# Optimization experiments

Hardware: AMD Instinct MI355X
Metric: run time of the kernel (lower is better)

## Reference

```python
import jax, jax.numpy as jnp
import numpy as np

N_NODES = 50000
IN_C = 128
OUT_C = 128
N_EDGES = 1600000
NEG_SLOPE = 0.2
EPS = 1e-16  # matches torch_geometric softmax denominator epsilon


def setup_inputs() -> dict:
    key = jax.random.key(0)
    k1, k2, k3, k4, k5 = jax.random.split(key, 5)
    glorot = 1.0 / np.sqrt(IN_C)
    x = jax.random.normal(k1, (N_NODES, IN_C), dtype=jnp.float32)
    W = jax.random.normal(k2, (IN_C, OUT_C), dtype=jnp.float32) * glorot
    a_src = jax.random.normal(k3, (OUT_C,), dtype=jnp.float32) * glorot
    a_dst = jax.random.normal(k4, (OUT_C,), dtype=jnp.float32) * glorot
    bias = jnp.zeros((OUT_C,), dtype=jnp.float32)
    edge_index = jax.random.randint(k5, (2, N_EDGES), 0, N_NODES, dtype=jnp.int32)
    return {"x": x, "W": W, "a_src": a_src, "a_dst": a_dst,
            "bias": bias, "edge_index": edge_index}


def reference(x, W, a_src, a_dst, bias, edge_index):
    N = x.shape[0]
    # add self loops (GATConv default add_self_loops=True)
    loops = jnp.arange(N, dtype=edge_index.dtype)
    src = jnp.concatenate([edge_index[0], loops])  # [E+N]
    dst = jnp.concatenate([edge_index[1], loops])

    h = x @ W                                      # [N, out]
    alpha_s = h @ a_src                            # [N]
    alpha_d = h @ a_dst                            # [N]

    e = alpha_s[src] + alpha_d[dst]                # [E+N]
    e = jnp.where(e > 0, e, NEG_SLOPE * e)         # leaky_relu

    # neighbor-wise (per destination node) stable softmax
    m = jax.ops.segment_max(e, dst, num_segments=N)
    ex = jnp.exp(e - m[dst])
    denom = jax.ops.segment_sum(ex, dst, num_segments=N)
    alpha = ex / (denom[dst] + EPS)

    # weighted aggregation of source features into destination nodes
    msgs = h[src] * alpha[:, None]                 # [E+N, out]
    out = jax.ops.segment_sum(msgs, dst, num_segments=N) + bias
    return jax.nn.relu(out)
```

## Files before the change

kernel.cpp:

```cpp
#include <hip/hip_runtime.h>
#include <hip/hip_fp16.h>

#define C 128
#define NEG_SLOPE 0.2f
#define SM_EPS 1e-16f
#define BKT_SHIFT 8
#define BKT_MASK 255
#define BIN_CHUNK 8192
#define WP 136

typedef unsigned int uint32;
typedef __attribute__((ext_vector_type(8))) short bf16x8;
typedef __attribute__((ext_vector_type(4))) float f32x4;

static __device__ __forceinline__ unsigned short f2bf(float f) {
    uint32 u = __float_as_uint(f);
    uint32 r = 0x7FFFu + ((u >> 16) & 1u);
    return (unsigned short)((u + r) >> 16);
}
static __device__ __forceinline__ uint32 f2bf2(float lo, float hi) {
    return (uint32)f2bf(lo) | ((uint32)f2bf(hi) << 16);
}
static __device__ __forceinline__ uint32 f2h(float f) {
    __half h = __float2half(f);
    return (uint32)*reinterpret_cast<unsigned short*>(&h);
}
static __device__ __forceinline__ float h2f(uint32 b) {
    unsigned short s = (unsigned short)(b & 0xffffu);
    __half h = *reinterpret_cast<__half*>(&s);
    return __half2float(h);
}

__global__ __launch_bounds__(256) void cvtw_kernel(const float* __restrict__ W,
                                                   uint32* __restrict__ Wf,
                                                   int* __restrict__ bucket_cnt,
                                                   int* __restrict__ bucket_progress, int NB) {
    int gid = blockIdx.x * 256 + threadIdx.x;
    if (blockIdx.x == 0 && threadIdx.x < NB) {
        bucket_cnt[threadIdx.x] = 0;
        bucket_progress[threadIdx.x] = 0;
    }
    int j2   = gid & 3;
    int lane = (gid >> 2) & 63;
    int tile = gid >> 8;
    int t = tile >> 2, kk = tile & 3;
    int n = t * 16 + (lane & 15);
    int k = kk * 32 + (lane >> 4) * 8 + j2 * 2;
    Wf[gid] = f2bf2(W[k * C + n], W[(k + 1) * C + n]);
}

__global__ __launch_bounds__(256) void gemm_hist_kernel(
    const float* __restrict__ x, const uint32* __restrict__ Wf,
    const float* __restrict__ a_src, const float* __restrict__ a_dst,
    unsigned short* __restrict__ hb, float* __restrict__ as_out,
    float* __restrict__ ad_out, int N,
    const int* __restrict__ dst, int* __restrict__ bucket_cnt, int E, int total, int NB)
{
    __shared__ __align__(16) unsigned short slice[4][16 * WP];
    __shared__ int bhist[256];

    const int tid  = threadIdx.x;
    const int lane = tid & 63;
    const int w    = tid >> 6;
    const int row0 = blockIdx.x * 64;
    const int m16  = lane & 15;
    const int q    = lane >> 4;

    bhist[tid] = 0;

    const int row = row0 + w * 16 + m16;
    const bool rv = (row < N);
    const float* xr_p = x + (size_t)(rv ? row : 0) * C + q * 8;

    float4 xr[8];
    #pragma unroll
    for (int kk = 0; kk < 4; ++kk) {
        xr[kk * 2]     = rv ? *(const float4*)(xr_p + kk * 32)     : make_float4(0, 0, 0, 0);
        xr[kk * 2 + 1] = rv ? *(const float4*)(xr_p + kk * 32 + 4) : make_float4(0, 0, 0, 0);
    }

    f32x4 acc[8];
    const f32x4 zz = {0.f, 0.f, 0.f, 0.f};
    #pragma unroll
    for (int t = 0; t < 8; ++t) acc[t] = zz;

    #pragma unroll
    for (int kk = 0; kk < 4; ++kk) {
        union { bf16x8 v; uint32 u[4]; } au;
        float4 p0 = xr[kk * 2], p1 = xr[kk * 2 + 1];
        au.u[0] = f2bf2(p0.x, p0.y); au.u[1] = f2bf2(p0.z, p0.w);
        au.u[2] = f2bf2(p1.x, p1.y); au.u[3] = f2bf2(p1.z, p1.w);
        #pragma unroll
        for (int t = 0; t < 8; ++t) {
            bf16x8 b = *(const bf16x8*)&Wf[((t * 4 + kk) * 64 + lane) * 4];
            acc[t] = __builtin_amdgcn_mfma_f32_16x16x32_bf16(au.v, b, acc[t], 0, 0, 0);
        }
    }

    float ps[4] = {0.f, 0.f, 0.f, 0.f}, pd[4] = {0.f, 0.f, 0.f, 0.f};
    #pragma unroll
    for (int t = 0; t < 8; ++t) {
        float av = a_src[t * 16 + m16];
        float dv = a_dst[t * 16 + m16];
        #pragma unroll
        for (int r = 0; r < 4; ++r) {
            ps[r] += acc[t][r] * av;
            pd[r] += acc[t][r] * dv;
        }
    }
    #pragma unroll
    for (int r = 0; r < 4; ++r) {
        #pragma unroll
        for (int off = 1; off < 16; off <<= 1) {
            ps[r] += __shfl_xor(ps[r], off, 64);
            pd[r] += __shfl_xor(pd[r], off, 64);
        }
    }
    if (m16 == 0) {
        #pragma unroll
        for (int r = 0; r < 4; ++r) {
            int rr = row0 + w * 16 + q * 4 + r;
            if (rr < N) { as_out[rr] = ps[r]; ad_out[rr] = pd[r]; }
        }
    }

    #pragma unroll
    for (int t = 0; t < 8; ++t)
        #pragma unroll
        for (int r = 0; r < 4; ++r)
            slice[w][(q * 4 + r) * WP + t * 16 + m16] = f2bf(acc[t][r]);
    __syncthreads();
    #pragma unroll
    for (int it = 0; it < 4; ++it) {
        int r = it * 4 + q;
        int rr = row0 + w * 16 + r;
        if (rr < N) {
            bf16x8 v = *(const bf16x8*)&slice[w][r * WP + m16 * 8];
            *(bf16x8*)&hb[(size_t)rr * C + m16 * 8] = v;
        }
    }

    for (int i = blockIdx.x * 256 + tid; i < total; i += gridDim.x * 256) {
        int d = (i < E) ? dst[i] : (i - E);
        atomicAdd(&bhist[d >> BKT_SHIFT], 1);
    }
    __syncthreads();
    if (tid < NB && bhist[tid]) atomicAdd(&bucket_cnt[tid], bhist[tid]);
}

__global__ __launch_bounds__(1024) void bin_kernel(
    const int* __restrict__ src, const int* __restrict__ dst,
    const int* __restrict__ bucket_cnt, int* __restrict__ bucket_progress,
    uint32* __restrict__ packed, int E, int total, int NB)
{
    __shared__ uint32 lsrc[BIN_CHUNK];
    __shared__ unsigned short ldst[BIN_CHUNK];
    __shared__ int hist[256];
    __shared__ int base[256];
    __shared__ int boff[256];
    __shared__ int wave_tot[4];
    const int tid = threadIdx.x;
    const int start = blockIdx.x * BIN_CHUNK;
    const int end = min(start + BIN_CHUNK, total);
    const int n = end - start;

    int v = 0, xx = 0;
    if (tid < 256) {
        hist[tid] = 0;
        const int lane = tid & 63;
        v = (tid < NB) ? bucket_cnt[tid] : 0;
        xx = v;
        #pragma unroll
        for (int o = 1; o < 64; o <<= 1) {
            int t = __shfl_up(xx, o, 64);
            if (lane >= o) xx += t;
        }
        if (lane == 63) wave_tot[tid >> 6] = xx;
    }
    for (int i = start + tid; i < end; i += 1024) {
        int s = (i < E) ? src[i] : (i - E);
        int d = (i < E) ? dst[i] : (i - E);
        lsrc[i - start] = (uint32)s;
        ldst[i - start] = (unsigned short)d;
    }
    __syncthreads();
    if (tid < 256) {
        const int wid = tid >> 6;
        int wbase = 0;
        #pragma unroll
        for (int w = 0; w < 4; ++w) wbase += (w < wid) ? wave_tot[w] : 0;
        boff[tid] = wbase + xx - v;
    }
    __syncthreads();
    for (int j = tid; j < n; j += 1024)
        atomicAdd(&hist[ldst[j] >> BKT_SHIFT], 1);
    __syncthreads();
    if (tid < NB) {
        int c = hist[tid];
        base[tid] = boff[tid] + (c ? atomicAdd(&bucket_progress[tid], c) : 0);
    }
    if (tid < 256) hist[tid] = 0;
    __syncthreads();
    for (int j = tid; j < n; j += 1024) {
        int d = ldst[j];
        int b = d >> BKT_SHIFT;
        int pos = base[b] + atomicAdd(&hist[b], 1);
        packed[pos] = (lsrc[j] << BKT_SHIFT) | (uint32)(d & BKT_MASK);
    }
}

__global__ __launch_bounds__(1024) void build_kernel(
    const uint32* __restrict__ packed, const int* __restrict__ bucket_cnt,
    const float* __restrict__ as, const float* __restrict__ ad,
    int* __restrict__ row_start, uint32* __restrict__ csr, int N, int NB, int total)
{
    __shared__ int cnt[256];
    __shared__ int cur[256];
    __shared__ float adl[256];
    __shared__ int boff[256];
    __shared__ int wave_tot[8];
    const int tid = threadIdx.x;
    const int b = blockIdx.x;

    int v = 0, xx = 0;
    if (tid < 256) {
        const int lane = tid & 63;
        v = (tid < NB) ? bucket_cnt[tid] : 0;
        xx = v;
        #pragma unroll
        for (int o = 1; o < 64; o <<= 1) {
            int t = __shfl_up(xx, o, 64);
            if (lane >= o) xx += t;
        }
        if (lane == 63) wave_tot[tid >> 6] = xx;
        cnt[tid] = 0;
        int g = (b << BKT_SHIFT) + tid;
        adl[tid] = (g < N) ? ad[g] : 0.f;
    }
    __syncthreads();
    if (tid < 256) {
        const int wid = tid >> 6;
        int wbase = 0;
        #pragma unroll
        for (int w = 0; w < 4; ++w) wbase += (w < wid) ? wave_tot[w] : 0;
        boff[tid] = wbase + xx - v;
    }
    __syncthreads();
    const int off = boff[b];
    const int end = off + ((b < NB) ? bucket_cnt[b] : 0);
    if (b == 0 && tid == 0) row_start[N] = total;

    for (int j = off + tid; j < end; j += 1024)
        atomicAdd(&cnt[packed[j] & BKT_MASK], 1);
    __syncthreads();

    int v2 = 0, x2 = 0;
    if (tid < 256) {
        const int lane = tid & 63;
        v2 = cnt[tid]; x2 = v2;
        #pragma unroll
        for (int o = 1; o < 64; o <<= 1) {
            int t = __shfl_up(x2, o, 64);
            if (lane >= o) x2 += t;
        }
        if (lane == 63) wave_tot[4 + (tid >> 6)] = x2;
    }
    __syncthreads();
    if (tid < 256) {
        const int wid = tid >> 6;
        int wbase = 0;
        #pragma unroll
        for (int w = 0; w < 4; ++w) wbase += (w < wid) ? wave_tot[4 + w] : 0;
        int excl = wbase + x2 - v2;
        int g = (b << BKT_SHIFT) + tid;
        if (g < N) row_start[g] = off + excl;
        cur[tid] = excl;
    }
    __syncthreads();

    for (int j = off + tid; j < end; j += 1024) {
        uint32 p = packed[j];
        int l = (int)(p & BKT_MASK);
        int s = (int)(p >> BKT_SHIFT);
        float e = as[s] + adl[l];
        e = (e > 0.f) ? e : NEG_SLOPE * e;
        int pos = atomicAdd(&cur[l], 1);
        csr[off + pos] = ((uint32)s << 16) | f2h(e);
    }
}

static __device__ __forceinline__ void gather_node_fw(
    int d, const uint32* __restrict__ csr, const int* __restrict__ row_start,
    const unsigned short* __restrict__ hb, const float* __restrict__ bias,
    float* __restrict__ out, int lane)
{
    const int beg = row_start[d];
    const int deg = row_start[d + 1] - beg;
    const int c2 = lane << 1;
    float a0 = 0.f, a1 = 0.f;
    float m = -INFINITY;
    for (int t = lane; t < deg; t += 64) m = fmaxf(m, h2f(csr[beg + t]));
    #pragma unroll
    for (int off = 32; off > 0; off >>= 1) m = fmaxf(m, __shfl_xor(m, off, 64));
    float ssum = 0.f;
    for (int t = lane; t < deg; t += 64) ssum += __expf(h2f(csr[beg + t]) - m);
    #pragma unroll
    for (int off = 32; off > 0; off >>= 1) ssum += __shfl_xor(ssum, off, 64);
    float inv = 1.f / (ssum + SM_EPS);
    for (int t0 = 0; t0 < deg; t0 += 64) {
        int nc = min(64, deg - t0);
        uint32 ent = (lane < nc) ? csr[beg + t0 + lane] : 0xFC00u;
        float wl = (lane < nc) ? __expf(h2f(ent) - m) * inv : 0.f;
        uint32 bc = (ent & 0xffff0000u) | f2h(wl);
        for (int t = 0; t < nc; ++t) {
            uint32 b0 = (uint32)__shfl((int)bc, t, 64);
            uint32 u0 = *(const uint32*)&hb[(size_t)(b0 >> 16) * C + c2];
            float w0 = h2f(b0);
            a0 += __uint_as_float(u0 << 16) * w0;
            a1 += __uint_as_float(u0 & 0xffff0000u) * w0;
        }
    }
    float2 b2 = *(const float2*)&bias[c2];
    a0 = fmaxf(a0 + b2.x, 0.f);
    a1 = fmaxf(a1 + b2.y, 0.f);
    *(float2*)&out[(size_t)d * C + c2] = make_float2(a0, a1);
}

#define EDGE_FMA(bc_reg, idx)                                                     \
    {                                                                             \
        uint32 bE = (uint32)__shfl((int)(bc_reg), hbase + (idx), 64);             \
        uint2 uE = *(const uint2*)&hb[(size_t)(bE >> 16) * C + c4];               \
        float wE = h2f(bE);                                                       \
        a0 += __uint_as_float(uE.x << 16) * wE;                                   \
        a1 += __uint_as_float(uE.x & 0xffff0000u) * wE;                           \
        a2 += __uint_as_float(uE.y << 16) * wE;                                   \
        a3 += __uint_as_float(uE.y & 0xffff0000u) * wE;                           \
    }

__global__ __launch_bounds__(256) void gather_kernel(
    const uint32* __restrict__ csr, const int* __restrict__ row_start,
    const unsigned short* __restrict__ hb, const float* __restrict__ bias,
    float* __restrict__ out, int N)
{
    const int w    = threadIdx.x >> 6;
    const int lane = threadIdx.x & 63;
    const int half = lane >> 5;
    const int hl   = lane & 31;
    const int pair = blockIdx.x * 4 + w;
    const int d0 = pair * 2;
    if (d0 >= N) return;
    const int d = d0 + half;
    const bool valid = (d < N);

    int beg = 0, deg = 0;
    if (valid) { beg = row_start[d]; deg = row_start[d + 1] - beg; }

    int wdeg = deg;
    #pragma unroll
    for (int off = 32; off > 0; off >>= 1) wdeg = max(wdeg, __shfl_xor(wdeg, off, 64));

    if (wdeg > 64) {
        gather_node_fw(d0, csr, row_start, hb, bias, out, lane);
        if (d0 + 1 < N) gather_node_fw(d0 + 1, csr, row_start, hb, bias, out, lane);
        return;
    }

    uint32 ent0 = (hl < deg) ? csr[beg + hl] : 0xFC00u;
    uint32 ent1 = (32 + hl < deg) ? csr[beg + 32 + hl] : 0xFC00u;
    float e0 = h2f(ent0), e1 = h2f(ent1);
    float m = fmaxf(e0, e1);
    #pragma unroll
    for (int off = 16; off > 0; off >>= 1) m = fmaxf(m, __shfl_xor(m, off, 64));
    float p0 = (hl < deg) ? __expf(e0 - m) : 0.f;
    float p1 = (32 + hl < deg) ? __expf(e1 - m) : 0.f;
    float ssum = p0 + p1;
    #pragma unroll
    for (int off = 16; off > 0; off >>= 1) ssum += __shfl_xor(ssum, off, 64);
    const float inv = 1.f / (ssum + SM_EPS);
    uint32 bc0 = (hl < deg) ? ((ent0 & 0xffff0000u) | f2h(p0 * inv)) : 0u;
    uint32 bc1 = (32 + hl < deg) ? ((ent1 & 0xffff0000u) | f2h(p1 * inv)) : 0u;

    const int c4 = hl << 2;
    const int hbase = half << 5;
    float a0 = 0.f, a1 = 0.f, a2 = 0.f, a3 = 0.f;

    const int n1 = min(deg, 32);
    int t = 0;
    for (; t + 8 <= n1; t += 8) {
        EDGE_FMA(bc0, t)     EDGE_FMA(bc0, t + 1) EDGE_FMA(bc0, t + 2) EDGE_FMA(bc0, t + 3)
        EDGE_FMA(bc0, t + 4) EDGE_FMA(bc0, t + 5) EDGE_FMA(bc0, t + 6) EDGE_FMA(bc0, t + 7)
    }
    for (; t < n1; ++t) { EDGE_FMA(bc0, t) }
    for (t = 32; t + 8 <= deg; t += 8) {
        EDGE_FMA(bc1, t - 32) EDGE_FMA(bc1, t - 31) EDGE_FMA(bc1, t - 30) EDGE_FMA(bc1, t - 29)
        EDGE_FMA(bc1, t - 28) EDGE_FMA(bc1, t - 27) EDGE_FMA(bc1, t - 26) EDGE_FMA(bc1, t - 25)
    }
    for (; t < deg; ++t) { EDGE_FMA(bc1, t - 32) }

    if (valid) {
        float4 bb = *(const float4*)&bias[c4];
        float4 o;
        o.x = fmaxf(a0 + bb.x, 0.f);
        o.y = fmaxf(a1 + bb.y, 0.f);
        o.z = fmaxf(a2 + bb.z, 0.f);
        o.w = fmaxf(a3 + bb.w, 0.f);
        *(float4*)&out[(size_t)d * C + c4] = o;
    }
}

extern "C" void kernel_launch(void* const* d_in, const int* in_sizes, int n_in,
                              void* d_out, int out_size, void* d_ws, size_t ws_size,
                              hipStream_t stream) {
    const float* x     = (const float*)d_in[0];
    const float* W     = (const float*)d_in[1];
    const float* a_src = (const float*)d_in[2];
    const float* a_dst = (const float*)d_in[3];
    const float* bias  = (const float*)d_in[4];
    const int*   edge  = (const int*)d_in[5];

    const int N = in_sizes[0] / C;
    const int E = in_sizes[5] / 2;
    const int total = E + N;
    const int* src = edge;
    const int* dst = edge + E;
    float* out = (float*)d_out;

    const int NB = (N + BKT_MASK) >> BKT_SHIFT;

    float* ws = (float*)d_ws;
    unsigned short* hb = (unsigned short*)ws;
    float* as = (float*)(hb + (size_t)N * C);
    float* ad = as + N;
    int* row_start       = (int*)(ad + N);
    uint32* packed       = (uint32*)(row_start + (N + 2));
    uint32* csr          = packed + total;
    uint32* Wf           = csr + total;
    int* bucket_cnt      = (int*)(Wf + 8192);
    int* bucket_progress = bucket_cnt + NB;

    cvtw_kernel<<<32, 256, 0, stream>>>(W, Wf, bucket_cnt, bucket_progress, NB);
    gemm_hist_kernel<<<(N + 63) / 64, 256, 0, stream>>>(
        x, Wf, a_src, a_dst, hb, as, ad, N, dst, bucket_cnt, E, total, NB);
    bin_kernel<<<(total + BIN_CHUNK - 1) / BIN_CHUNK, 1024, 0, stream>>>(
        src, dst, bucket_cnt, bucket_progress, packed, E, total, NB);
    build_kernel<<<NB, 1024, 0, stream>>>(packed, bucket_cnt, as, ad, row_start,
                                          csr, N, NB, total);
    gather_kernel<<<((N + 1) / 2 + 3) / 4, 256, 0, stream>>>(csr, row_start, hb, bias, out, N);
}
```

Baseline: 205.9 us.

## Fuse GEMM, binning, CSR build and gather into one persistent kernel

Replaces the four kernel launches after weight conversion with a single persistent mega_kernel of 256 blocks × 1024 threads. The phases (GEMM plus histogram, binning, CSR build, gather) are separated by software grid barriers that spin on atomic counters. The aim is to remove launch gaps and tail effects between stages, and the gather now strides over pairs with a fixed set of waves. In exchange it relies on all blocks being co-resident, since the barriers would deadlock otherwise. It may also lose occupancy in the latency-bound gather, or spill registers under the new launch bounds.

```diff
diff --git a/kernel.cpp b/kernel.cpp
--- a/kernel.cpp
+++ b/kernel.cpp
@@ -8,6 +8,8 @@
 #define BKT_MASK 255
 #define BIN_CHUNK 8192
 #define WP 136
+#define GRID 256
+#define BT 1024
 
 typedef unsigned int uint32;
 typedef __attribute__((ext_vector_type(8))) short bf16x8;
@@ -34,11 +36,12 @@
 __global__ __launch_bounds__(256) void cvtw_kernel(const float* __restrict__ W,
                                                    uint32* __restrict__ Wf,
                                                    int* __restrict__ bucket_cnt,
-                                                   int* __restrict__ bucket_progress, int NB) {
+                                                   int* __restrict__ bucket_progress,
+                                                   int* __restrict__ bar, int NB) {
     int gid = blockIdx.x * 256 + threadIdx.x;
-    if (blockIdx.x == 0 && threadIdx.x < NB) {
-        bucket_cnt[threadIdx.x] = 0;
-        bucket_progress[threadIdx.x] = 0;
+    if (blockIdx.x == 0) {
+        if (threadIdx.x < NB) { bucket_cnt[threadIdx.x] = 0; bucket_progress[threadIdx.x] = 0; }
+        if (threadIdx.x < 8) bar[threadIdx.x] = 0;
     }
     int j2   = gid & 3;
     int lane = (gid >> 2) & 63;
@@ -49,244 +52,16 @@
     Wf[gid] = f2bf2(W[k * C + n], W[(k + 1) * C + n]);
 }
 
-__global__ __launch_bounds__(256) void gemm_hist_kernel(
-    const float* __restrict__ x, const uint32* __restrict__ Wf,
-    const float* __restrict__ a_src, const float* __restrict__ a_dst,
-    unsigned short* __restrict__ hb, float* __restrict__ as_out,
-    float* __restrict__ ad_out, int N,
-    const int* __restrict__ dst, int* __restrict__ bucket_cnt, int E, int total, int NB)
-{
-    __shared__ __align__(16) unsigned short slice[4][16 * WP];
-    __shared__ int bhist[256];
-
-    const int tid  = threadIdx.x;
-    const int lane = tid & 63;
-    const int w    = tid >> 6;
-    const int row0 = blockIdx.x * 64;
-    const int m16  = lane & 15;
-    const int q    = lane >> 4;
-
-    bhist[tid] = 0;
-
-    const int row = row0 + w * 16 + m16;
-    const bool rv = (row < N);
-    const float* xr_p = x + (size_t)(rv ? row : 0) * C + q * 8;
-
-    float4 xr[8];
-    #pragma unroll
-    for (int kk = 0; kk < 4; ++kk) {
-        xr[kk * 2]     = rv ? *(const float4*)(xr_p + kk * 32)     : make_float4(0, 0, 0, 0);
-        xr[kk * 2 + 1] = rv ? *(const float4*)(xr_p + kk * 32 + 4) : make_float4(0, 0, 0, 0);
-    }
-
-    f32x4 acc[8];
-    const f32x4 zz = {0.f, 0.f, 0.f, 0.f};
-    #pragma unroll
-    for (int t = 0; t < 8; ++t) acc[t] = zz;
-
-    #pragma unroll
-    for (int kk = 0; kk < 4; ++kk) {
-        union { bf16x8 v; uint32 u[4]; } au;
-        float4 p0 = xr[kk * 2], p1 = xr[kk * 2 + 1];
-        au.u[0] = f2bf2(p0.x, p0.y); au.u[1] = f2bf2(p0.z, p0.w);
-        au.u[2] = f2bf2(p1.x, p1.y); au.u[3] = f2bf2(p1.z, p1.w);
-        #pragma unroll
-        for (int t = 0; t < 8; ++t) {
-            bf16x8 b = *(const bf16x8*)&Wf[((t * 4 + kk) * 64 + lane) * 4];
-            acc[t] = __builtin_amdgcn_mfma_f32_16x16x32_bf16(au.v, b, acc[t], 0, 0, 0);
-        }
-    }
-
-    float ps[4] = {0.f, 0.f, 0.f, 0.f}, pd[4] = {0.f, 0.f, 0.f, 0.f};
-    #pragma unroll
-    for (int t = 0; t < 8; ++t) {
-        float av = a_src[t * 16 + m16];
-        float dv = a_dst[t * 16 + m16];
-        #pragma unroll
-        for (int r = 0; r < 4; ++r) {
-            ps[r] += acc[t][r] * av;
-            pd[r] += acc[t][r] * dv;
-        }
-    }
-    #pragma unroll
-    for (int r = 0; r < 4; ++r) {
-        #pragma unroll
-        for (int off = 1; off < 16; off <<= 1) {
-            ps[r] += __shfl_xor(ps[r], off, 64);
-            pd[r] += __shfl_xor(pd[r], off, 64);
-        }
-    }
-    if (m16 == 0) {
-        #pragma unroll
-        for (int r = 0; r < 4; ++r) {
-            int rr = row0 + w * 16 + q * 4 + r;
-            if (rr < N) { as_out[rr] = ps[r]; ad_out[rr] = pd[r]; }
-        }
-    }
-
-    #pragma unroll
-    for (int t = 0; t < 8; ++t)
-        #pragma unroll
-        for (int r = 0; r < 4; ++r)
-            slice[w][(q * 4 + r) * WP + t * 16 + m16] = f2bf(acc[t][r]);
+static __device__ __forceinline__ void gbar(int* __restrict__ bar, int idx) {
     __syncthreads();
-    #pragma unroll
-    for (int it = 0; it < 4; ++it) {
-        int r = it * 4 + q;
-        int rr = row0 + w * 16 + r;
-        if (rr < N) {
-            bf16x8 v = *(const bf16x8*)&slice[w][r * WP + m16 * 8];
-            *(bf16x8*)&hb[(size_t)rr * C + m16 * 8] = v;
-        }
-    }
-
-    for (int i = blockIdx.x * 256 + tid; i < total; i += gridDim.x * 256) {
-        int d = (i < E) ? dst[i] : (i - E);
-        atomicAdd(&bhist[d >> BKT_SHIFT], 1);
+    if (threadIdx.x == 0) {
+        __threadfence();
+        atomicAdd(&bar[idx], 1);
+        while (atomicAdd(&bar[idx], 0) < (int)gridDim.x)
+            __builtin_amdgcn_s_sleep(1);
+        __threadfence();
     }
     __syncthreads();
-    if (tid < NB && bhist[tid]) atomicAdd(&bucket_cnt[tid], bhist[tid]);
-}
-
-__global__ __launch_bounds__(1024) void bin_kernel(
-    const int* __restrict__ src, const int* __restrict__ dst,
-    const int* __restrict__ bucket_cnt, int* __restrict__ bucket_progress,
-    uint32* __restrict__ packed, int E, int total, int NB)
-{
-    __shared__ uint32 lsrc[BIN_CHUNK];
-    __shared__ unsigned short ldst[BIN_CHUNK];
-    __shared__ int hist[256];
-    __shared__ int base[256];
-    __shared__ int boff[256];
-    __shared__ int wave_tot[4];
-    const int tid = threadIdx.x;
-    const int start = blockIdx.x * BIN_CHUNK;
-    const int end = min(start + BIN_CHUNK, total);
-    const int n = end - start;
-
-    int v = 0, xx = 0;
-    if (tid < 256) {
-        hist[tid] = 0;
-        const int lane = tid & 63;
-        v = (tid < NB) ? bucket_cnt[tid] : 0;
-        xx = v;
-        #pragma unroll
-        for (int o = 1; o < 64; o <<= 1) {
-            int t = __shfl_up(xx, o, 64);
-            if (lane >= o) xx += t;
-        }
-        if (lane == 63) wave_tot[tid >> 6] = xx;
-    }
-    for (int i = start + tid; i < end; i += 1024) {
-        int s = (i < E) ? src[i] : (i - E);
-        int d = (i < E) ? dst[i] : (i - E);
-        lsrc[i - start] = (uint32)s;
-        ldst[i - start] = (unsigned short)d;
-    }
-    __syncthreads();
-    if (tid < 256) {
-        const int wid = tid >> 6;
-        int wbase = 0;
-        #pragma unroll
-        for (int w = 0; w < 4; ++w) wbase += (w < wid) ? wave_tot[w] : 0;
-        boff[tid] = wbase + xx - v;
-    }
-    __syncthreads();
-    for (int j = tid; j < n; j += 1024)
-        atomicAdd(&hist[ldst[j] >> BKT_SHIFT], 1);
-    __syncthreads();
-    if (tid < NB) {
-        int c = hist[tid];
-        base[tid] = boff[tid] + (c ? atomicAdd(&bucket_progress[tid], c) : 0);
-    }
-    if (tid < 256) hist[tid] = 0;
-    __syncthreads();
-    for (int j = tid; j < n; j += 1024) {
-        int d = ldst[j];
-        int b = d >> BKT_SHIFT;
-        int pos = base[b] + atomicAdd(&hist[b], 1);
-        packed[pos] = (lsrc[j] << BKT_SHIFT) | (uint32)(d & BKT_MASK);
-    }
-}
-
-__global__ __launch_bounds__(1024) void build_kernel(
-    const uint32* __restrict__ packed, const int* __restrict__ bucket_cnt,
-    const float* __restrict__ as, const float* __restrict__ ad,
-    int* __restrict__ row_start, uint32* __restrict__ csr, int N, int NB, int total)
-{
-    __shared__ int cnt[256];
-    __shared__ int cur[256];
-    __shared__ float adl[256];
-    __shared__ int boff[256];
-    __shared__ int wave_tot[8];
-    const int tid = threadIdx.x;
-    const int b = blockIdx.x;
-
-    int v = 0, xx = 0;
-    if (tid < 256) {
-        const int lane = tid & 63;
-        v = (tid < NB) ? bucket_cnt[tid] : 0;
-        xx = v;
-        #pragma unroll
-        for (int o = 1; o < 64; o <<= 1) {
-            int t = __shfl_up(xx, o, 64);
-            if (lane >= o) xx += t;
-        }
-        if (lane == 63) wave_tot[tid >> 6] = xx;
-        cnt[tid] = 0;
-        int g = (b << BKT_SHIFT) + tid;
-        adl[tid] = (g < N) ? ad[g] : 0.f;
-    }
-    __syncthreads();
-    if (tid < 256) {
-        const int wid = tid >> 6;
-        int wbase = 0;
-        #pragma unroll
-        for (int w = 0; w < 4; ++w) wbase += (w < wid) ? wave_tot[w] : 0;
-        boff[tid] = wbase + xx - v;
-    }
-    __syncthreads();
-    const int off = boff[b];
-    const int end = off + ((b < NB) ? bucket_cnt[b] : 0);
-    if (b == 0 && tid == 0) row_start[N] = total;
-
-    for (int j = off + tid; j < end; j += 1024)
-        atomicAdd(&cnt[packed[j] & BKT_MASK], 1);
-    __syncthreads();
-
-    int v2 = 0, x2 = 0;
-    if (tid < 256) {
-        const int lane = tid & 63;
-        v2 = cnt[tid]; x2 = v2;
-        #pragma unroll
-        for (int o = 1; o < 64; o <<= 1) {
-            int t = __shfl_up(x2, o, 64);
-            if (lane >= o) x2 += t;
-        }
-        if (lane == 63) wave_tot[4 + (tid >> 6)] = x2;
-    }
-    __syncthreads();
-    if (tid < 256) {
-        const int wid = tid >> 6;
-        int wbase = 0;
-        #pragma unroll
-        for (int w = 0; w < 4; ++w) wbase += (w < wid) ? wave_tot[4 + w] : 0;
-        int excl = wbase + x2 - v2;
-        int g = (b << BKT_SHIFT) + tid;
-        if (g < N) row_start[g] = off + excl;
-        cur[tid] = excl;
-    }
-    __syncthreads();
-
-    for (int j = off + tid; j < end; j += 1024) {
-        uint32 p = packed[j];
-        int l = (int)(p & BKT_MASK);
-        int s = (int)(p >> BKT_SHIFT);
-        float e = as[s] + adl[l];
-        e = (e > 0.f) ? e : NEG_SLOPE * e;
-        int pos = atomicAdd(&cur[l], 1);
-        csr[off + pos] = ((uint32)s << 16) | f2h(e);
-    }
 }
 
 static __device__ __forceinline__ void gather_node_fw(
@@ -321,9 +96,8 @@
         }
     }
     float2 b2 = *(const float2*)&bias[c2];
-    a0 = fmaxf(a0 + b2.x, 0.f);
-    a1 = fmaxf(a1 + b2.y, 0.f);
-    *(float2*)&out[(size_t)d * C + c2] = make_float2(a0, a1);
+    *(float2*)&out[(size_t)d * C + c2] =
+        make_float2(fmaxf(a0 + b2.x, 0.f), fmaxf(a1 + b2.y, 0.f));
 }
 
 #define EDGE_FMA(bc_reg, idx)                                                     \
@@ -337,18 +111,13 @@
         a3 += __uint_as_float(uE.y & 0xffff0000u) * wE;                           \
     }
 
-__global__ __launch_bounds__(256) void gather_kernel(
-    const uint32* __restrict__ csr, const int* __restrict__ row_start,
+static __device__ __forceinline__ void gather_pair(
+    int d0, const uint32* __restrict__ csr, const int* __restrict__ row_start,
     const unsigned short* __restrict__ hb, const float* __restrict__ bias,
-    float* __restrict__ out, int N)
+    float* __restrict__ out, int N, int lane)
 {
-    const int w    = threadIdx.x >> 6;
-    const int lane = threadIdx.x & 63;
     const int half = lane >> 5;
     const int hl   = lane & 31;
-    const int pair = blockIdx.x * 4 + w;
-    const int d0 = pair * 2;
-    if (d0 >= N) return;
     const int d = d0 + half;
     const bool valid = (d < N);
 
@@ -408,6 +177,257 @@
     }
 }
 
+__global__ __launch_bounds__(BT, 4) void mega_kernel(
+    const float* __restrict__ x, const uint32* __restrict__ Wf,
+    const float* __restrict__ a_src, const float* __restrict__ a_dst,
+    unsigned short* __restrict__ hb, float* __restrict__ as,
+    float* __restrict__ ad, const int* __restrict__ src, const int* __restrict__ dst,
+    int* __restrict__ bucket_cnt, int* __restrict__ bucket_progress,
+    uint32* __restrict__ packed, uint32* __restrict__ csr,
+    int* __restrict__ row_start, const float* __restrict__ bias,
+    float* __restrict__ out, int* __restrict__ bar,
+    int N, int E, int total, int NB)
+{
+    __shared__ __align__(16) unsigned char smem[69664];
+    __shared__ int wave_tot[8];
+    const int tid = threadIdx.x;
+
+    {
+        const int qd   = tid >> 8;
+        const int lane = tid & 63;
+        const int wq   = (tid >> 6) & 3;
+        const int m16  = lane & 15;
+        const int q    = lane >> 4;
+        const int ntiles = (N + 63) >> 6;
+        const int tile = blockIdx.x * 4 + qd;
+        const bool tv = (tile < ntiles);
+        const int row0 = tile << 6;
+        unsigned short* slice = (unsigned short*)smem + (size_t)(qd * 4 + wq) * 16 * WP;
+
+        if (tv) {
+            const int row = row0 + wq * 16 + m16;
+            const bool rv = (row < N);
+            const float* xr_p = x + (size_t)(rv ? row : 0) * C + q * 8;
+            float4 xr[8];
+            #pragma unroll
+            for (int kk = 0; kk < 4; ++kk) {
+                xr[kk * 2]     = rv ? *(const float4*)(xr_p + kk * 32)     : make_float4(0, 0, 0, 0);
+                xr[kk * 2 + 1] = rv ? *(const float4*)(xr_p + kk * 32 + 4) : make_float4(0, 0, 0, 0);
+            }
+            f32x4 acc[8];
+            const f32x4 zz = {0.f, 0.f, 0.f, 0.f};
+            #pragma unroll
+            for (int t = 0; t < 8; ++t) acc[t] = zz;
+            #pragma unroll
+            for (int kk = 0; kk < 4; ++kk) {
+                union { bf16x8 v; uint32 u[4]; } au;
+                float4 p0 = xr[kk * 2], p1 = xr[kk * 2 + 1];
+                au.u[0] = f2bf2(p0.x, p0.y); au.u[1] = f2bf2(p0.z, p0.w);
+                au.u[2] = f2bf2(p1.x, p1.y); au.u[3] = f2bf2(p1.z, p1.w);
+                #pragma unroll
+                for (int t = 0; t < 8; ++t) {
+                    bf16x8 b = *(const bf16x8*)&Wf[((t * 4 + kk) * 64 + lane) * 4];
+                    acc[t] = __builtin_amdgcn_mfma_f32_16x16x32_bf16(au.v, b, acc[t], 0, 0, 0);
+                }
+            }
+            float ps[4] = {0.f, 0.f, 0.f, 0.f}, pd[4] = {0.f, 0.f, 0.f, 0.f};
+            #pragma unroll
+            for (int t = 0; t < 8; ++t) {
+                float av = a_src[t * 16 + m16];
+                float dv = a_dst[t * 16 + m16];
+                #pragma unroll
+                for (int r = 0; r < 4; ++r) { ps[r] += acc[t][r] * av; pd[r] += acc[t][r] * dv; }
+            }
+            #pragma unroll
+            for (int r = 0; r < 4; ++r) {
+                #pragma unroll
+                for (int off = 1; off < 16; off <<= 1) {
+                    ps[r] += __shfl_xor(ps[r], off, 64);
+                    pd[r] += __shfl_xor(pd[r], off, 64);
+                }
+            }
+            if (m16 == 0) {
+                #pragma unroll
+                for (int r = 0; r < 4; ++r) {
+                    int rr = row0 + wq * 16 + q * 4 + r;
+                    if (rr < N) { as[rr] = ps[r]; ad[rr] = pd[r]; }
+                }
+            }
+            #pragma unroll
+            for (int t = 0; t < 8; ++t)
+                #pragma unroll
+                for (int r = 0; r < 4; ++r)
+                    slice[(q * 4 + r) * WP + t * 16 + m16] = f2bf(acc[t][r]);
+        }
+        __syncthreads();
+        if (tv) {
+            #pragma unroll
+            for (int it = 0; it < 4; ++it) {
+                int r = it * 4 + q;
+                int rr = row0 + wq * 16 + r;
+                if (rr < N) {
+                    bf16x8 v = *(const bf16x8*)&slice[r * WP + m16 * 8];
+                    *(bf16x8*)&hb[(size_t)rr * C + m16 * 8] = v;
+                }
+            }
+        }
+        __syncthreads();
+        int* bhist = (int*)smem;
+        if (tid < 256) bhist[tid] = 0;
+        __syncthreads();
+        for (int i = blockIdx.x * BT + tid; i < total; i += gridDim.x * BT) {
+            int d = (i < E) ? dst[i] : (i - E);
+            atomicAdd(&bhist[d >> BKT_SHIFT], 1);
+        }
+        __syncthreads();
+        if (tid < NB && bhist[tid]) atomicAdd(&bucket_cnt[tid], bhist[tid]);
+    }
+    gbar(bar, 0);
+
+    {
+        const int nchunks = (total + BIN_CHUNK - 1) / BIN_CHUNK;
+        if ((int)blockIdx.x < nchunks) {
+            uint32* lsrc = (uint32*)smem;
+            unsigned short* ldst = (unsigned short*)(smem + 32768);
+            int* hist = (int*)(smem + 49152);
+            int* base = (int*)(smem + 50176);
+            int* boff = (int*)(smem + 51200);
+            const int start = blockIdx.x * BIN_CHUNK;
+            const int end = min(start + BIN_CHUNK, total);
+            const int n = end - start;
+
+            int v = 0, xx = 0;
+            if (tid < 256) {
+                hist[tid] = 0;
+                const int lane = tid & 63;
+                v = (tid < NB) ? bucket_cnt[tid] : 0;
+                xx = v;
+                #pragma unroll
+                for (int o = 1; o < 64; o <<= 1) {
+                    int t = __shfl_up(xx, o, 64);
+                    if (lane >= o) xx += t;
+                }
+                if (lane == 63) wave_tot[tid >> 6] = xx;
+            }
+            for (int i = start + tid; i < end; i += BT) {
+                lsrc[i - start] = (uint32)((i < E) ? src[i] : (i - E));
+                ldst[i - start] = (unsigned short)((i < E) ? dst[i] : (i - E));
+            }
+            __syncthreads();
+            if (tid < 256) {
+                const int wid = tid >> 6;
+                int wbase = 0;
+                #pragma unroll
+                for (int w = 0; w < 4; ++w) wbase += (w < wid) ? wave_tot[w] : 0;
+                boff[tid] = wbase + xx - v;
+            }
+            __syncthreads();
+            for (int j = tid; j < n; j += BT)
+                atomicAdd(&hist[ldst[j] >> BKT_SHIFT], 1);
+            __syncthreads();
+            if (tid < NB) {
+                int c = hist[tid];
+                base[tid] = boff[tid] + (c ? atomicAdd(&bucket_progress[tid], c) : 0);
+            }
+            if (tid < 256) hist[tid] = 0;
+            __syncthreads();
+            for (int j = tid; j < n; j += BT) {
+                int d = ldst[j];
+                int b = d >> BKT_SHIFT;
+                int pos = base[b] + atomicAdd(&hist[b], 1);
+                packed[pos] = (lsrc[j] << BKT_SHIFT) | (uint32)(d & BKT_MASK);
+            }
+        }
+    }
+    gbar(bar, 1);
+
+    {
+        const int b = blockIdx.x;
+        if (b == 0 && tid == 0) row_start[N] = total;
+        if (b < NB) {
+            int* cnt   = (int*)smem;
+            int* cur   = (int*)(smem + 1024);
+            float* adl = (float*)(smem + 2048);
+            int* boff  = (int*)(smem + 3072);
+
+            int v = 0, xx = 0;
+            if (tid < 256) {
+                const int lane = tid & 63;
+                v = (tid < NB) ? bucket_cnt[tid] : 0;
+                xx = v;
+                #pragma unroll
+                for (int o = 1; o < 64; o <<= 1) {
+                    int t = __shfl_up(xx, o, 64);
+                    if (lane >= o) xx += t;
+                }
+                if (lane == 63) wave_tot[tid >> 6] = xx;
+                cnt[tid] = 0;
+                int g = (b << BKT_SHIFT) + tid;
+                adl[tid] = (g < N) ? ad[g] : 0.f;
+            }
+            __syncthreads();
+            if (tid < 256) {
+                const int wid = tid >> 6;
+                int wbase = 0;
+                #pragma unroll
+                for (int w = 0; w < 4; ++w) wbase += (w < wid) ? wave_tot[w] : 0;
+                boff[tid] = wbase + xx - v;
+            }
+            __syncthreads();
+            const int off = boff[b & 255];
+            const int end = off + bucket_cnt[b];
+
+            for (int j = off + tid; j < end; j += BT)
+                atomicAdd(&cnt[packed[j] & BKT_MASK], 1);
+            __syncthreads();
+
+            int v2 = 0, x2 = 0;
+            if (tid < 256) {
+                const int lane = tid & 63;
+                v2 = cnt[tid]; x2 = v2;
+                #pragma unroll
+                for (int o = 1; o < 64; o <<= 1) {
+                    int t = __shfl_up(x2, o, 64);
+                    if (lane >= o) x2 += t;
+                }
+                if (lane == 63) wave_tot[4 + (tid >> 6)] = x2;
+            }
+            __syncthreads();
+            if (tid < 256) {
+                const int wid = tid >> 6;
+                int wbase = 0;
+                #pragma unroll
+                for (int w = 0; w < 4; ++w) wbase += (w < wid) ? wave_tot[4 + w] : 0;
+                int excl = wbase + x2 - v2;
+                int g = (b << BKT_SHIFT) + tid;
+                if (g < N) row_start[g] = off + excl;
+                cur[tid] = excl;
+            }
+            __syncthreads();
+
+            for (int j = off + tid; j < end; j += BT) {
+                uint32 p = packed[j];
+                int l = (int)(p & BKT_MASK);
+                int s = (int)(p >> BKT_SHIFT);
+                float e = as[s] + adl[l];
+                e = (e > 0.f) ? e : NEG_SLOPE * e;
+                int pos = atomicAdd(&cur[l], 1);
+                csr[off + pos] = ((uint32)s << 16) | f2h(e);
+            }
+        }
+    }
+    gbar(bar, 2);
+
+    {
+        const int lane = tid & 63;
+        const int gw = blockIdx.x * (BT / 64) + (tid >> 6);
+        const int nwaves = gridDim.x * (BT / 64);
+        const int npairs = (N + 1) / 2;
+        for (int p = gw; p < npairs; p += nwaves)
+            gather_pair(p * 2, csr, row_start, hb, bias, out, N, lane);
+    }
+}
+
 extern "C" void kernel_launch(void* const* d_in, const int* in_sizes, int n_in,
                               void* d_out, int out_size, void* d_ws, size_t ws_size,
                               hipStream_t stream) {
@@ -437,13 +457,11 @@
     uint32* Wf           = csr + total;
     int* bucket_cnt      = (int*)(Wf + 8192);
     int* bucket_progress = bucket_cnt + NB;
-
-    cvtw_kernel<<<32, 256, 0, stream>>>(W, Wf, bucket_cnt, bucket_progress, NB);
-    gemm_hist_kernel<<<(N + 63) / 64, 256, 0, stream>>>(
-        x, Wf, a_src, a_dst, hb, as, ad, N, dst, bucket_cnt, E, total, NB);
-    bin_kernel<<<(total + BIN_CHUNK - 1) / BIN_CHUNK, 1024, 0, stream>>>(
-        src, dst, bucket_cnt, bucket_progress, packed, E, total, NB);
-    build_kernel<<<NB, 1024, 0, stream>>>(packed, bucket_cnt, as, ad, row_start,
-                                          csr, N, NB, total);
-    gather_kernel<<<((N + 1) / 2 + 3) / 4, 256, 0, stream>>>(csr, row_start, hb, bias, out, N);
-}
+    int* bar             = bucket_progress + NB;
+
+    cvtw_kernel<<<32, 256, 0, stream>>>(W, Wf, bucket_cnt, bucket_progress, bar, NB);
+    mega_kernel<<<GRID, BT, 0, stream>>>(
+        x, Wf, a_src, a_dst, hb, as, ad, src, dst,
+        bucket_cnt, bucket_progress, packed, csr, row_start,
+        bias, out, bar, N, E, total, NB);
+}
```

After: 283.9 us. +37.9%, slower.
